# Optimization experiments

Hardware: AMD Instinct MI355X
Metric: run time of the kernel (lower is better)

Reference implementation:

```python
import jax, jax.numpy as jnp
import numpy as np

H = 256  # hidden_size
I = 18   # input_size
B = 1024 # batch
T = 1024 # seq_len


def setup_inputs() -> dict:
    key = jax.random.key(0)
    ks = jax.random.split(key, 8)
    scale = 1.0 / np.sqrt(H)  # matches torch GRUCell uniform init scale roughly
    s = lambda k, shape: jax.random.normal(k, shape, dtype=jnp.float32) * scale
    return {
        "x": jax.random.normal(ks[0], (B, T, I), dtype=jnp.float32),
        # layer 0 GRUCell params (gate order r, z, n as in torch)
        "W_ih0": s(ks[1], (3 * H, I)),
        "W_hh0": s(ks[2], (3 * H, H)),
        "b_ih0": jnp.zeros((3 * H,), dtype=jnp.float32),
        "b_hh0": jnp.zeros((3 * H,), dtype=jnp.float32),
        # layer 1 GRUCell params
        "W_ih1": s(ks[3], (3 * H, H)),
        "W_hh1": s(ks[4], (3 * H, H)),
        "b_ih1": jnp.zeros((3 * H,), dtype=jnp.float32),
        "b_hh1": jnp.zeros((3 * H,), dtype=jnp.float32),
        "fc_w": s(ks[5], (1, H)),
        "fc_b": jnp.zeros((1,), dtype=jnp.float32),
    }


def _gru_cell(x, h, W_ih, W_hh, b_ih, b_hh):
    # torch.nn.GRUCell math, gate order (r, z, n)
    gi = x @ W_ih.T + b_ih  # (B, 3H)
    gh = h @ W_hh.T + b_hh  # (B, 3H)
    ir, iz, inn = jnp.split(gi, 3, axis=-1)
    hr, hz, hn = jnp.split(gh, 3, axis=-1)
    r = jax.nn.sigmoid(ir + hr)
    z = jax.nn.sigmoid(iz + hz)
    n = jnp.tanh(inn + r * hn)
    return (1.0 - z) * n + z * h


def reference(x, W_ih0, W_hh0, b_ih0, b_hh0, W_ih1, W_hh1, b_ih1, b_hh1, fc_w, fc_b):
    batch = x.shape[0]
    hid = W_hh0.shape[1]
    h_init = (jnp.zeros((batch, hid), dtype=x.dtype),
              jnp.zeros((batch, hid), dtype=x.dtype))
    xs = jnp.swapaxes(x, 0, 1)  # (T, B, I) for scan over time

    def step(carry, xt):
        h0, h1 = carry
        h0 = _gru_cell(xt, h0, W_ih0, W_hh0, b_ih0, b_hh0)
        h1 = _gru_cell(h0, h1, W_ih1, W_hh1, b_ih1, b_hh1)
        return (h0, h1), None

    (h0, h1), _ = jax.lax.scan(step, h_init, xs)
    return h1 @ fc_w.T + fc_b  # (B, 1)
```

## Files before the change

kernel.cpp:

```cpp
#include <hip/hip_runtime.h>

#define B_ 1024
#define T_ 1024
#define I_ 18
#define H_ 256
#define NCHUNK 16
#define NSLICE 16

typedef _Float16 f16;
typedef _Float16 f16x8 __attribute__((ext_vector_type(8)));
typedef float f32x4 __attribute__((ext_vector_type(4)));

#define MFMA16(a, b, c) __builtin_amdgcn_mfma_f32_16x16x32_f16((a), (b), (c), 0, 0, 0)
#define SB() __builtin_amdgcn_sched_barrier(0)

#define H_SLOT (NCHUNK * 8 * 4 * 512)
#define NFLAGS (NCHUNK * 4 * 32)

struct TrueT { static constexpr bool value = true; };
struct FalseT { static constexpr bool value = false; };

__device__ __forceinline__ int hoff(int chunk, int kt, int m) {
  return (((chunk * 8) + kt) * 4 + m) * 512;
}

__global__ void init_ws(f16* __restrict__ hb, int* __restrict__ flg) {
  int i = blockIdx.x * blockDim.x + threadIdx.x;
  unsigned* p = (unsigned*)hb;
  for (int k = i; k < 3 * H_SLOT; k += gridDim.x * blockDim.x) p[k] = 0u;
  if (i < NFLAGS + 256 + 1) flg[i] = 0;
}

__device__ __forceinline__ float sigm(float v) {
  return __builtin_amdgcn_rcpf(1.f + __expf(-v));
}
__device__ __forceinline__ float tanh_fast(float v) {
  v = fmaxf(v, -15.f);
  float e = __expf(-2.f * v);
  return (1.f - e) * __builtin_amdgcn_rcpf(1.f + e);
}
__device__ __forceinline__ f16x8 cvt8(const float* q) {
  const f32x4* a = (const f32x4*)q;
  f32x4 u = a[0], v = a[1];
  f16x8 r;
  r[0] = (f16)u[0]; r[1] = (f16)u[1]; r[2] = (f16)u[2]; r[3] = (f16)u[3];
  r[4] = (f16)v[0]; r[5] = (f16)v[1]; r[6] = (f16)v[2]; r[7] = (f16)v[3];
  return r;
}

template <bool FAST>
__device__ __forceinline__ f16x8 ldh(const f16* p) {
  f16x8 r;
  if (FAST)
    asm volatile("global_load_dwordx4 %0, %1, off nt" : "=&v"(r) : "v"(p));
  else
    asm volatile("global_load_dwordx4 %0, %1, off sc0 sc1" : "=&v"(r) : "v"(p));
  return r;
}
template <bool FAST>
__device__ __forceinline__ void sth(f16* p, f16 v) {
  unsigned u = (unsigned)__builtin_bit_cast(unsigned short, v);
  if (FAST)
    asm volatile("global_store_short %0, %1, off" ::"v"(p), "v"(u) : "memory");
  else
    asm volatile("global_store_short %0, %1, off sc0 sc1" ::"v"(p), "v"(u)
                 : "memory");
}
template <bool FAST>
__device__ __forceinline__ void stf(int* p, int v) {
  if (FAST)
    asm volatile("global_store_dword %0, %1, off" ::"v"(p), "v"(v) : "memory");
  else
    asm volatile("global_store_dword %0, %1, off sc0 sc1" ::"v"(p), "v"(v)
                 : "memory");
}
template <bool FAST>
__device__ __forceinline__ int ldf(const int* p) {
  int r;
  if (FAST)
    asm volatile("global_load_dword %0, %1, off nt\n\ts_waitcnt vmcnt(0)"
                 : "=&v"(r) : "v"(p) : "memory");
  else
    asm volatile("global_load_dword %0, %1, off sc0 sc1\n\ts_waitcnt vmcnt(0)"
                 : "=&v"(r) : "v"(p) : "memory");
  return r;
}
__device__ __forceinline__ int ld_sys(const int* p) {
  int r;
  asm volatile("global_load_dword %0, %1, off sc0 sc1\n\ts_waitcnt vmcnt(0)"
               : "=&v"(r) : "v"(p) : "memory");
  return r;
}
__device__ __forceinline__ void st_sys(int* p, int v) { stf<false>(p, v); }
__device__ __forceinline__ f32x4 ldx4(const float* p) {
  f32x4 r;
  asm volatile("global_load_dwordx4 %0, %1, off" : "=&v"(r) : "v"(p));
  return r;
}

__global__ __launch_bounds__(512, 2) void gru_main(
    const float* __restrict__ x, const float* __restrict__ Wih0,
    const float* __restrict__ Whh0, const float* __restrict__ Wih1,
    const float* __restrict__ Whh1, const float* __restrict__ bih0,
    const float* __restrict__ bhh0, const float* __restrict__ bih1,
    const float* __restrict__ bhh1, const float* __restrict__ fcw,
    f16* __restrict__ hb0, f16* __restrict__ hb1, float* __restrict__ part,
    int* __restrict__ flags, int* __restrict__ ids, int* __restrict__ dec) {
  __shared__ f16 whh1_l[24 * 512];

  const int tid = threadIdx.x;
  const int wv = tid >> 6, lane = tid & 63;
  const int w = wv & 3;
  const bool isL0 = wv < 4;
  const int lrow = lane & 15, lgrp = lane >> 4;
  const int chunk = blockIdx.x & 15, slice = blockIdx.x >> 4;
  const int c = slice * 16 + lrow;

  for (int idx = tid; idx < 24 * 64; idx += 512) {
    int f = idx >> 6, l = idx & 63;
    int g = f >> 3, kt = f & 7;
    int n = g * H_ + slice * 16 + (l & 15);
    ((f16x8*)whh1_l)[idx] = cvt8(&Whh1[n * H_ + kt * 32 + (l >> 4) * 8]);
  }

  const int* fpoll = flags + (chunk * 4 + w) * 32 + (lane & 31);
  const int rbase = chunk * 64 + w * 16;
  const int s_kt = slice >> 1;
  const int s_off = 128 * ((slice & 1) * 2 + (lrow >> 3)) + (lrow & 7);

  {
    unsigned xcc;
    asm volatile("s_getreg_b32 %0, hwreg(HW_REG_XCC_ID)" : "=s"(xcc));
    if (tid == 0) st_sys(ids + blockIdx.x, (int)xcc + 1);
    if (blockIdx.x == 0 && wv == 0) {
      int ok, guard = 0;
      for (;;) {
        int v0 = ld_sys(ids + lane * 4 + 0), v1 = ld_sys(ids + lane * 4 + 1);
        int v2 = ld_sys(ids + lane * 4 + 2), v3 = ld_sys(ids + lane * 4 + 3);
        ok = (v0 && v1 && v2 && v3);
        if (__all(ok)) { ok = 1; break; }
        if (++guard > (1 << 16)) { ok = 0; break; }
        __builtin_amdgcn_s_sleep(8);
      }
      int verdict = 1;
      if (ok) {
        int eq = 1;
        if (lane < 16) {
          int r0 = ld_sys(ids + lane);
          for (int s = 1; s < 16; ++s)
            eq &= (ld_sys(ids + s * 16 + lane) == r0);
        }
        verdict = __all(eq) ? 2 : 1;
      }
      if (lane == 0) st_sys(dec, verdict);
    }
  }
  int decision = 1;
  {
    int g = 0;
    for (;;) {
      int d = ld_sys(dec);
      if (d) { decision = d; break; }
      if (++g > (1 << 20)) break;
      __builtin_amdgcn_s_sleep(8);
    }
  }
  __syncthreads();

  if (isL0) {
    f16x8 wfA[27];
#pragma unroll
    for (int g = 0; g < 3; ++g) {
      int n = g * H_ + c;
      f16 v[8];
#pragma unroll
      for (int j = 0; j < 8; ++j) {
        int k = lgrp * 8 + j;
        v[j] = (k < I_) ? (f16)Wih0[n * I_ + k] : (f16)0.f;
      }
      wfA[g] = *(f16x8*)v;
    }
#pragma unroll
    for (int g = 0; g < 3; ++g)
#pragma unroll
      for (int kt = 0; kt < 8; ++kt)
        wfA[3 + g * 8 + kt] =
            cvt8(&Whh0[(g * H_ + c) * H_ + kt * 32 + lgrp * 8]);

    const float bR0 = bih0[c] + bhh0[c], bZ0 = bih0[H_ + c] + bhh0[H_ + c];
    const float bI0 = bih0[2 * H_ + c], bH0 = bhh0[2 * H_ + c];
    float h0r[4] = {0.f, 0.f, 0.f, 0.f};
    int* fpost0 = flags + (chunk * 4 + w) * 32 + slice;
    const float* xrow = x + (size_t)(rbase + lrow) * T_ * I_;
    const int o1 = (lgrp == 0) ? 0 : (lgrp == 1) ? 8 : (lgrp == 2) ? 14 : 0;
    const int o2 = (lgrp == 0) ? 4 : (lgrp == 1) ? 12 : 0;
    int dead = 0;

    auto loop0 = [&](auto FC) {
      constexpr bool F = decltype(FC)::value;
      asm volatile("s_waitcnt vmcnt(0)" ::: "memory");
      SB();
      f32x4 xA1 = ldx4(xrow + o1);
      f32x4 xA2 = ldx4(xrow + o2);
      asm volatile("s_waitcnt vmcnt(0)" ::: "memory");
      SB();
      for (int p = 0; p < T_; ++p) {
        __builtin_amdgcn_s_setprio(1);
        if (p > 0 && !dead) {
          int guard = 0;
          for (;;) {
            int v = ldf<F>(fpoll);
            int tgt = (lane & 16) ? (p - 3) : p;
            if (__all(v >= tgt)) break;
            if (++guard > (1 << 18)) { dead = 1; break; }
          }
        }
        SB();
        f16x8 ah0[8];
        {
          const f16* b0 = hb0 + (size_t)((p - 1) & 3) * H_SLOT +
                          hoff(chunk, 0, w) + lane * 8;
#pragma unroll
          for (int kt = 0; kt < 8; ++kt) ah0[kt] = ldh<F>(b0 + kt * 2048);
        }
        SB();
        f16x8 ax;
        {
          float s0 = (lgrp == 2) ? xA1[2] : xA1[0];
          float s1 = (lgrp == 2) ? xA1[3] : xA1[1];
          ax[0] = (f16)s0;     ax[1] = (f16)s1;
          ax[2] = (f16)xA1[2]; ax[3] = (f16)xA1[3];
          ax[4] = (f16)xA2[0]; ax[5] = (f16)xA2[1];
          ax[6] = (f16)xA2[2]; ax[7] = (f16)xA2[3];
        }
        f32x4 aR = {bR0, bR0, bR0, bR0}, aZ = {bZ0, bZ0, bZ0, bZ0};
        f32x4 aI = {bI0, bI0, bI0, bI0}, aH = {bH0, bH0, bH0, bH0};
        aR = MFMA16(ax, wfA[0], aR);
        aZ = MFMA16(ax, wfA[1], aZ);
        aI = MFMA16(ax, wfA[2], aI);
        SB();
        asm volatile("s_waitcnt vmcnt(4)" ::: "memory");
        SB();
#pragma unroll
        for (int kt = 0; kt < 4; ++kt) {
          aR = MFMA16(ah0[kt], wfA[3 + kt], aR);
          aZ = MFMA16(ah0[kt], wfA[11 + kt], aZ);
          aH = MFMA16(ah0[kt], wfA[19 + kt], aH);
        }
        SB();
        asm volatile("s_waitcnt vmcnt(0)" ::: "memory");
        SB();
#pragma unroll
        for (int kt = 4; kt < 8; ++kt) {
          aR = MFMA16(ah0[kt], wfA[3 + kt], aR);
          aZ = MFMA16(ah0[kt], wfA[11 + kt], aZ);
          aH = MFMA16(ah0[kt], wfA[19 + kt], aH);
        }
        {
          f16* d0 = hb0 + (size_t)(p & 3) * H_SLOT + hoff(chunk, s_kt, w) +
                    s_off;
#pragma unroll
          for (int i = 0; i < 4; ++i) {
            float rr = sigm(aR[i]);
            float zz = sigm(aZ[i]);
            float nn = tanh_fast(aI[i] + rr * aH[i]);
            h0r[i] = (1.f - zz) * nn + zz * h0r[i];
            sth<F>(d0 + (lgrp * 4 + i) * 8, (f16)h0r[i]);
          }
        }
        {
          int tn = (p + 1 < T_) ? p + 1 : T_ - 1;
          const float* px = xrow + (size_t)tn * I_;
          xA1 = ldx4(px + o1);
          xA2 = ldx4(px + o2);
        }
        SB();
        asm volatile("s_waitcnt vmcnt(2)" ::: "memory");
        SB();
        if (lane == 0) stf<F>(fpost0, p + 1);
        __builtin_amdgcn_s_setprio(0);
      }
    };
    if (decision == 2) loop0(TrueT{});
    else loop0(FalseT{});
  } else {
    f16x8 wfB[24];
#pragma unroll
    for (int g = 0; g < 3; ++g)
#pragma unroll
      for (int kt = 0; kt < 8; ++kt)
        wfB[g * 8 + kt] =
            cvt8(&Wih1[(g * H_ + c) * H_ + kt * 32 + lgrp * 8]);

    const float bR1 = bih1[c] + bhh1[c], bZ1 = bih1[H_ + c] + bhh1[H_ + c];
    const float bI1 = bih1[2 * H_ + c], bH1 = bhh1[2 * H_ + c];
    const float fw = fcw[c];
    float h1r[4] = {0.f, 0.f, 0.f, 0.f};
    int* fpost1 = flags + (chunk * 4 + w) * 32 + 16 + slice;
    int dead = 0;

    auto loop1 = [&](auto FC) {
      constexpr bool F = decltype(FC)::value;
      for (int p = 1; p <= T_; ++p) {
        if (!dead) {
          int guard = 0;
          for (;;) {
            int v = ldf<F>(fpoll);
            if (__all((lane & 16) ? (v >= p - 1) : 1)) break;
            if (++guard > (1 << 18)) { dead = 1; break; }
          }
        }
        SB();
        f16x8 ah1[8];
        {
          const f16* b1 = hb1 + (size_t)(p & 1) * H_SLOT +
                          hoff(chunk, 0, w) + lane * 8;
#pragma unroll
          for (int kt = 0; kt < 8; ++kt) ah1[kt] = ldh<F>(b1 + kt * 2048);
        }
        SB();
        if (!dead) {
          int guard = 0;
          for (;;) {
            int v = ldf<F>(fpoll);
            if (__all((lane & 16) ? 1 : (v >= p))) break;
            if (++guard > (1 << 18)) { dead = 1; break; }
          }
        }
        SB();
        f16x8 ah0[8];
        {
          const f16* b0 = hb0 + (size_t)((p - 1) & 3) * H_SLOT +
                          hoff(chunk, 0, w) + lane * 8;
#pragma unroll
          for (int kt = 0; kt < 8; ++kt) ah0[kt] = ldh<F>(b0 + kt * 2048);
        }
        SB();
        f32x4 aR = {bR1, bR1, bR1, bR1}, aZ = {bZ1, bZ1, bZ1, bZ1};
        f32x4 aI = {bI1, bI1, bI1, bI1}, aH = {bH1, bH1, bH1, bH1};
#pragma unroll
        for (int kt = 0; kt < 8; ++kt) {
          f16x8 br = *(const f16x8*)&whh1_l[(0 * 8 + kt) * 512 + lane * 8];
          f16x8 bz = *(const f16x8*)&whh1_l[(1 * 8 + kt) * 512 + lane * 8];
          f16x8 bn = *(const f16x8*)&whh1_l[(2 * 8 + kt) * 512 + lane * 8];
          aR = MFMA16(ah1[kt], br, aR);
          aZ = MFMA16(ah1[kt], bz, aZ);
          aH = MFMA16(ah1[kt], bn, aH);
        }
        SB();
        asm volatile("s_waitcnt vmcnt(0)" ::: "memory");
        SB();
#pragma unroll
        for (int kt = 0; kt < 8; ++kt) {
          aR = MFMA16(ah0[kt], wfB[kt], aR);
          aZ = MFMA16(ah0[kt], wfB[8 + kt], aZ);
          aI = MFMA16(ah0[kt], wfB[16 + kt], aI);
        }
        {
          f16* d1 = hb1 + (size_t)((p - 1) & 1) * H_SLOT +
                    hoff(chunk, s_kt, w) + s_off;
#pragma unroll
          for (int i = 0; i < 4; ++i) {
            float rr = sigm(aR[i]);
            float zz = sigm(aZ[i]);
            float nn = tanh_fast(aI[i] + rr * aH[i]);
            h1r[i] = (1.f - zz) * nn + zz * h1r[i];
            sth<F>(d1 + (lgrp * 4 + i) * 8, (f16)h1r[i]);
          }
        }
        SB();
        asm volatile("s_waitcnt vmcnt(0)" ::: "memory");
        SB();
        if (lane == 0) stf<F>(fpost1, p);
      }
    };
    if (decision == 2) loop1(TrueT{});
    else loop1(FalseT{});

    float tmp[4];
#pragma unroll
    for (int i = 0; i < 4; ++i) {
      float v = h1r[i] * fw;
#pragma unroll
      for (int m = 1; m < 16; m <<= 1) v += __shfl_xor(v, m);
      tmp[i] = v;
    }
    if (lrow == 0) {
#pragma unroll
      for (int i = 0; i < 4; ++i)
        part[(size_t)(rbase + lgrp * 4 + i) * 16 + slice] = tmp[i];
    }
  }
}

__global__ void fc_reduce(const float* __restrict__ part,
                          const float* __restrict__ fcb,
                          float* __restrict__ out) {
  int r = blockIdx.x * blockDim.x + threadIdx.x;
  if (r < B_) {
    float s = fcb[0];
#pragma unroll
    for (int i = 0; i < 16; ++i) s += part[r * 16 + i];
    out[r] = s;
  }
}

extern "C" void kernel_launch(void* const* d_in, const int* in_sizes, int n_in,
                              void* d_out, int out_size, void* d_ws, size_t ws_size,
                              hipStream_t stream) {
  const float* x    = (const float*)d_in[0];
  const float* Wih0 = (const float*)d_in[1];
  const float* Whh0 = (const float*)d_in[2];
  const float* bih0 = (const float*)d_in[3];
  const float* bhh0 = (const float*)d_in[4];
  const float* Wih1 = (const float*)d_in[5];
  const float* Whh1 = (const float*)d_in[6];
  const float* bih1 = (const float*)d_in[7];
  const float* bhh1 = (const float*)d_in[8];
  const float* fcw  = (const float*)d_in[9];
  const float* fcb  = (const float*)d_in[10];

  f16* hb0 = (f16*)d_ws;
  f16* hb1 = hb0 + (size_t)4 * H_SLOT;
  float* part = (float*)(hb1 + (size_t)2 * H_SLOT);
  int* flags = (int*)(part + 1024 * 16);
  int* ids = flags + NFLAGS;
  int* dec = ids + 256;

  init_ws<<<1024, 256, 0, stream>>>(hb0, flags);
  gru_main<<<256, 512, 0, stream>>>(x, Wih0, Whh0, Wih1, Whh1, bih0, bhh0,
                                    bih1, bhh1, fcw, hb0, hb1, part, flags,
                                    ids, dec);
  fc_reduce<<<4, 256, 0, stream>>>(part, fcb, (float*)d_out);
}
```

Baseline: 1.905 ms.

## Split GRU into three pipelined stages with batch-chunked blocks and LDS-resident hidden state

Replaces the layer-0/layer-1 split over 16 batch chunks × 16 hidden slices with 192 blocks in three stages per 16-row batch chunk. Stage 0 runs the layer-0 recurrence, stage 1 the layer-1 input projection, stage 2 the layer-1 recurrence. Each block now owns the full hidden dimension for its batch rows. The recurrent hidden state stays in an LDS ring instead of being exchanged through global memory every step, and the recurrent weights are split between registers and LDS. Stages hand off through global ring buffers with flag-based credit flow control, and the FC head is fused into the last stage. This removes the per-step global h exchange and the separate reduction kernel, but adds inter-stage latency and leaves one block per CU with higher register pressure.

```diff
diff --git a/kernel.cpp b/kernel.cpp
--- a/kernel.cpp
+++ b/kernel.cpp
@@ -1,34 +1,26 @@
 #include <hip/hip_runtime.h>
 
-#define B_ 1024
 #define T_ 1024
 #define I_ 18
-#define H_ 256
-#define NCHUNK 16
-#define NSLICE 16
+#define NCH 64
+#define GUARD (1 << 18)
 
 typedef _Float16 f16;
 typedef _Float16 f16x8 __attribute__((ext_vector_type(8)));
+typedef _Float16 f16x4 __attribute__((ext_vector_type(4)));
 typedef float f32x4 __attribute__((ext_vector_type(4)));
 
 #define MFMA16(a, b, c) __builtin_amdgcn_mfma_f32_16x16x32_f16((a), (b), (c), 0, 0, 0)
 #define SB() __builtin_amdgcn_sched_barrier(0)
 
-#define H_SLOT (NCHUNK * 8 * 4 * 512)
-#define NFLAGS (NCHUNK * 4 * 32)
-
-struct TrueT { static constexpr bool value = true; };
-struct FalseT { static constexpr bool value = false; };
-
-__device__ __forceinline__ int hoff(int chunk, int kt, int m) {
-  return (((chunk * 8) + kt) * 4 + m) * 512;
-}
-
-__global__ void init_ws(f16* __restrict__ hb, int* __restrict__ flg) {
+#define HB0_ELEMS (4 * 64 * 4096)
+#define GB1_ELEMS (4 * 64 * 12288)
+#define NFLAGS (NCH * 32)
+#define LDS_BYTES 114688
+
+__global__ void init_ws(int* __restrict__ flg) {
   int i = blockIdx.x * blockDim.x + threadIdx.x;
-  unsigned* p = (unsigned*)hb;
-  for (int k = i; k < 3 * H_SLOT; k += gridDim.x * blockDim.x) p[k] = 0u;
-  if (i < NFLAGS + 256 + 1) flg[i] = 0;
+  if (i < NFLAGS + 192 + 1) flg[i] = 0;
 }
 
 __device__ __forceinline__ float sigm(float v) {
@@ -51,28 +43,31 @@
 template <bool FAST>
 __device__ __forceinline__ f16x8 ldh(const f16* p) {
   f16x8 r;
-  if (FAST)
-    asm volatile("global_load_dwordx4 %0, %1, off nt" : "=&v"(r) : "v"(p));
-  else
-    asm volatile("global_load_dwordx4 %0, %1, off sc0 sc1" : "=&v"(r) : "v"(p));
+  if (FAST) asm volatile("global_load_dwordx4 %0, %1, off nt" : "=&v"(r) : "v"(p));
+  else asm volatile("global_load_dwordx4 %0, %1, off sc0 sc1" : "=&v"(r) : "v"(p));
   return r;
 }
 template <bool FAST>
-__device__ __forceinline__ void sth(f16* p, f16 v) {
-  unsigned u = (unsigned)__builtin_bit_cast(unsigned short, v);
-  if (FAST)
-    asm volatile("global_store_short %0, %1, off" ::"v"(p), "v"(u) : "memory");
-  else
-    asm volatile("global_store_short %0, %1, off sc0 sc1" ::"v"(p), "v"(u)
-                 : "memory");
+__device__ __forceinline__ f16x4 ldg8(const f16* p) {
+  f16x4 r;
+  if (FAST) asm volatile("global_load_dwordx2 %0, %1, off nt" : "=&v"(r) : "v"(p));
+  else asm volatile("global_load_dwordx2 %0, %1, off sc0 sc1" : "=&v"(r) : "v"(p));
+  return r;
+}
+template <bool FAST>
+__device__ __forceinline__ void stg16(f16* p, f16x8 v) {
+  if (FAST) asm volatile("global_store_dwordx4 %0, %1, off" ::"v"(p), "v"(v) : "memory");
+  else asm volatile("global_store_dwordx4 %0, %1, off sc0 sc1" ::"v"(p), "v"(v) : "memory");
+}
+template <bool FAST>
+__device__ __forceinline__ void stg8(f16* p, f16x4 v) {
+  if (FAST) asm volatile("global_store_dwordx2 %0, %1, off" ::"v"(p), "v"(v) : "memory");
+  else asm volatile("global_store_dwordx2 %0, %1, off sc0 sc1" ::"v"(p), "v"(v) : "memory");
 }
 template <bool FAST>
 __device__ __forceinline__ void stf(int* p, int v) {
-  if (FAST)
-    asm volatile("global_store_dword %0, %1, off" ::"v"(p), "v"(v) : "memory");
-  else
-    asm volatile("global_store_dword %0, %1, off sc0 sc1" ::"v"(p), "v"(v)
-                 : "memory");
+  if (FAST) asm volatile("global_store_dword %0, %1, off" ::"v"(p), "v"(v) : "memory");
+  else asm volatile("global_store_dword %0, %1, off sc0 sc1" ::"v"(p), "v"(v) : "memory");
 }
 template <bool FAST>
 __device__ __forceinline__ int ldf(const int* p) {
@@ -85,6 +80,11 @@
                  : "=&v"(r) : "v"(p) : "memory");
   return r;
 }
+template <bool FAST>
+__device__ __forceinline__ void ldf_nw(const int* p, int* dst) {
+  if (FAST) asm volatile("global_load_dword %0, %1, off nt" : "=&v"(*dst) : "v"(p) : "memory");
+  else asm volatile("global_load_dword %0, %1, off sc0 sc1" : "=&v"(*dst) : "v"(p) : "memory");
+}
 __device__ __forceinline__ int ld_sys(const int* p) {
   int r;
   asm volatile("global_load_dword %0, %1, off sc0 sc1\n\ts_waitcnt vmcnt(0)"
@@ -98,35 +98,44 @@
   return r;
 }
 
-__global__ __launch_bounds__(512, 2) void gru_main(
+__global__ __launch_bounds__(512, 1) void gru_main(
     const float* __restrict__ x, const float* __restrict__ Wih0,
     const float* __restrict__ Whh0, const float* __restrict__ Wih1,
     const float* __restrict__ Whh1, const float* __restrict__ bih0,
     const float* __restrict__ bhh0, const float* __restrict__ bih1,
     const float* __restrict__ bhh1, const float* __restrict__ fcw,
-    f16* __restrict__ hb0, f16* __restrict__ hb1, float* __restrict__ part,
-    int* __restrict__ flags, int* __restrict__ ids, int* __restrict__ dec) {
-  __shared__ f16 whh1_l[24 * 512];
+    const float* __restrict__ fcb, f16* __restrict__ hb0,
+    f16* __restrict__ gb1, int* __restrict__ flags, int* __restrict__ ids,
+    int* __restrict__ dec, float* __restrict__ out) {
+  extern __shared__ f16 lds[];
+  f16* hring = lds + 96 * 512;
 
   const int tid = threadIdx.x;
   const int wv = tid >> 6, lane = tid & 63;
-  const int w = wv & 3;
-  const bool isL0 = wv < 4;
   const int lrow = lane & 15, lgrp = lane >> 4;
-  const int chunk = blockIdx.x & 15, slice = blockIdx.x >> 4;
-  const int c = slice * 16 + lrow;
-
-  for (int idx = tid; idx < 24 * 64; idx += 512) {
-    int f = idx >> 6, l = idx & 63;
-    int g = f >> 3, kt = f & 7;
-    int n = g * H_ + slice * 16 + (l & 15);
-    ((f16x8*)whh1_l)[idx] = cvt8(&Whh1[n * H_ + kt * 32 + (l >> 4) * 8]);
+  const int stage = blockIdx.x >> 6;
+  const int c = blockIdx.x & 63;
+
+  const float* Wm = (stage == 0) ? Whh0 : (stage == 1) ? Wih1 : Whh1;
+
+  for (int idx = tid; idx < 96 * 64; idx += 512) {
+    int f = idx >> 6, lf = idx & 63;
+    int nt = f >> 1, kk = 6 + (f & 1);
+    *(f16x8*)&lds[f * 512 + lf * 8] =
+        cvt8(&Wm[(nt * 16 + (lf & 15)) * 256 + kk * 32 + (lf >> 4) * 8]);
   }
-
-  const int* fpoll = flags + (chunk * 4 + w) * 32 + (lane & 31);
-  const int rbase = chunk * 64 + w * 16;
-  const int s_kt = slice >> 1;
-  const int s_off = 128 * ((slice & 1) * 2 + (lrow >> 3)) + (lrow & 7);
+  for (int idx = tid; idx < 2 * 4096; idx += 512) hring[idx] = (f16)0.f;
+
+  f16x8 wfr[36];
+#pragma unroll
+  for (int g = 0; g < 3; ++g)
+#pragma unroll
+    for (int tt = 0; tt < 2; ++tt) {
+      int row = g * 256 + 32 * wv + 16 * tt + lrow;
+#pragma unroll
+      for (int kt = 0; kt < 6; ++kt)
+        wfr[(g * 2 + tt) * 6 + kt] = cvt8(&Wm[row * 256 + kt * 32 + lgrp * 8]);
+    }
 
   {
     unsigned xcc;
@@ -135,21 +144,18 @@
     if (blockIdx.x == 0 && wv == 0) {
       int ok, guard = 0;
       for (;;) {
-        int v0 = ld_sys(ids + lane * 4 + 0), v1 = ld_sys(ids + lane * 4 + 1);
-        int v2 = ld_sys(ids + lane * 4 + 2), v3 = ld_sys(ids + lane * 4 + 3);
-        ok = (v0 && v1 && v2 && v3);
+        int v0 = ld_sys(ids + lane), v1 = ld_sys(ids + 64 + lane);
+        int v2 = ld_sys(ids + 128 + lane);
+        ok = (v0 && v1 && v2);
         if (__all(ok)) { ok = 1; break; }
         if (++guard > (1 << 16)) { ok = 0; break; }
         __builtin_amdgcn_s_sleep(8);
       }
       int verdict = 1;
       if (ok) {
-        int eq = 1;
-        if (lane < 16) {
-          int r0 = ld_sys(ids + lane);
-          for (int s = 1; s < 16; ++s)
-            eq &= (ld_sys(ids + s * 16 + lane) == r0);
-        }
+        int r0 = ld_sys(ids + lane), r1 = ld_sys(ids + 64 + lane);
+        int r2 = ld_sys(ids + 128 + lane);
+        int eq = (r1 == r0) && (r2 == r0);
         verdict = __all(eq) ? 2 : 1;
       }
       if (lane == 0) st_sys(dec, verdict);
@@ -167,62 +173,46 @@
   }
   __syncthreads();
 
-  if (isL0) {
-    f16x8 wfA[27];
-#pragma unroll
-    for (int g = 0; g < 3; ++g) {
-      int n = g * H_ + c;
-      f16 v[8];
-#pragma unroll
-      for (int j = 0; j < 8; ++j) {
-        int k = lgrp * 8 + j;
-        v[j] = (k < I_) ? (f16)Wih0[n * I_ + k] : (f16)0.f;
+  int dead = 0;
+
+  if (stage == 0) {
+    f16x8 wx[6];
+#pragma unroll
+    for (int g = 0; g < 3; ++g)
+#pragma unroll
+      for (int tt = 0; tt < 2; ++tt) {
+        int row = g * 256 + 32 * wv + 16 * tt + lrow;
+        f16 v[8];
+#pragma unroll
+        for (int j = 0; j < 8; ++j) {
+          int k = lgrp * 8 + j;
+          v[j] = (k < I_) ? (f16)Wih0[row * I_ + k] : (f16)0.f;
+        }
+        wx[g * 2 + tt] = *(f16x8*)v;
       }
-      wfA[g] = *(f16x8*)v;
-    }
-#pragma unroll
-    for (int g = 0; g < 3; ++g)
-#pragma unroll
-      for (int kt = 0; kt < 8; ++kt)
-        wfA[3 + g * 8 + kt] =
-            cvt8(&Whh0[(g * H_ + c) * H_ + kt * 32 + lgrp * 8]);
-
-    const float bR0 = bih0[c] + bhh0[c], bZ0 = bih0[H_ + c] + bhh0[H_ + c];
-    const float bI0 = bih0[2 * H_ + c], bH0 = bhh0[2 * H_ + c];
-    float h0r[4] = {0.f, 0.f, 0.f, 0.f};
-    int* fpost0 = flags + (chunk * 4 + w) * 32 + slice;
-    const float* xrow = x + (size_t)(rbase + lrow) * T_ * I_;
+    float bR[2], bZ[2], bI[2], bH[2];
+#pragma unroll
+    for (int tt = 0; tt < 2; ++tt) {
+      int col = 32 * wv + 16 * tt + lrow;
+      bR[tt] = bih0[col] + bhh0[col];
+      bZ[tt] = bih0[256 + col] + bhh0[256 + col];
+      bI[tt] = bih0[512 + col];
+      bH[tt] = bhh0[512 + col];
+    }
+    float h0r[2][4] = {{0.f, 0.f, 0.f, 0.f}, {0.f, 0.f, 0.f, 0.f}};
+    const float* xrow = x + (size_t)(c * 16 + lrow) * T_ * I_;
     const int o1 = (lgrp == 0) ? 0 : (lgrp == 1) ? 8 : (lgrp == 2) ? 14 : 0;
     const int o2 = (lgrp == 0) ? 4 : (lgrp == 1) ? 12 : 0;
-    int dead = 0;
+    int* fpost = flags + c * 32 + 0 * 8 + wv;
+    const int* fcred = flags + c * 32 + 2 * 8 + (lane & 7);
+    int cval = 0;
 
     auto loop0 = [&](auto FC) {
       constexpr bool F = decltype(FC)::value;
-      asm volatile("s_waitcnt vmcnt(0)" ::: "memory");
-      SB();
       f32x4 xA1 = ldx4(xrow + o1);
       f32x4 xA2 = ldx4(xrow + o2);
-      asm volatile("s_waitcnt vmcnt(0)" ::: "memory");
-      SB();
-      for (int p = 0; p < T_; ++p) {
-        __builtin_amdgcn_s_setprio(1);
-        if (p > 0 && !dead) {
-          int guard = 0;
-          for (;;) {
-            int v = ldf<F>(fpoll);
-            int tgt = (lane & 16) ? (p - 3) : p;
-            if (__all(v >= tgt)) break;
-            if (++guard > (1 << 18)) { dead = 1; break; }
-          }
-        }
-        SB();
-        f16x8 ah0[8];
-        {
-          const f16* b0 = hb0 + (size_t)((p - 1) & 3) * H_SLOT +
-                          hoff(chunk, 0, w) + lane * 8;
-#pragma unroll
-          for (int kt = 0; kt < 8; ++kt) ah0[kt] = ldh<F>(b0 + kt * 2048);
-        }
+      for (int t = 0; t < T_; ++t) {
+        asm volatile("s_waitcnt vmcnt(2)" ::: "memory");
         SB();
         f16x8 ax;
         {
@@ -233,175 +223,260 @@
           ax[4] = (f16)xA2[0]; ax[5] = (f16)xA2[1];
           ax[6] = (f16)xA2[2]; ax[7] = (f16)xA2[3];
         }
-        f32x4 aR = {bR0, bR0, bR0, bR0}, aZ = {bZ0, bZ0, bZ0, bZ0};
-        f32x4 aI = {bI0, bI0, bI0, bI0}, aH = {bH0, bH0, bH0, bH0};
-        aR = MFMA16(ax, wfA[0], aR);
-        aZ = MFMA16(ax, wfA[1], aZ);
-        aI = MFMA16(ax, wfA[2], aI);
-        SB();
-        asm volatile("s_waitcnt vmcnt(4)" ::: "memory");
-        SB();
-#pragma unroll
-        for (int kt = 0; kt < 4; ++kt) {
-          aR = MFMA16(ah0[kt], wfA[3 + kt], aR);
-          aZ = MFMA16(ah0[kt], wfA[11 + kt], aZ);
-          aH = MFMA16(ah0[kt], wfA[19 + kt], aH);
-        }
-        SB();
+        f32x4 aR[2], aZ[2], aI[2], aH[2];
+#pragma unroll
+        for (int tt = 0; tt < 2; ++tt) {
+          aR[tt] = (f32x4){bR[tt], bR[tt], bR[tt], bR[tt]};
+          aZ[tt] = (f32x4){bZ[tt], bZ[tt], bZ[tt], bZ[tt]};
+          aI[tt] = (f32x4){bI[tt], bI[tt], bI[tt], bI[tt]};
+          aH[tt] = (f32x4){bH[tt], bH[tt], bH[tt], bH[tt]};
+          aR[tt] = MFMA16(ax, wx[0 * 2 + tt], aR[tt]);
+          aZ[tt] = MFMA16(ax, wx[1 * 2 + tt], aZ[tt]);
+          aI[tt] = MFMA16(ax, wx[2 * 2 + tt], aI[tt]);
+        }
+        const f16* ha = &hring[((t + 1) & 1) * 4096 + lane * 8];
+#pragma unroll
+        for (int kt = 0; kt < 8; ++kt) {
+          f16x8 a = *(const f16x8*)(ha + kt * 512);
+#pragma unroll
+          for (int tt = 0; tt < 2; ++tt) {
+            f16x8 br = (kt < 6) ? wfr[(0 * 2 + tt) * 6 + kt]
+                : *(const f16x8*)&lds[(((0 * 16 + wv * 2 + tt) * 2) + (kt - 6)) * 512 + lane * 8];
+            f16x8 bz = (kt < 6) ? wfr[(1 * 2 + tt) * 6 + kt]
+                : *(const f16x8*)&lds[(((1 * 16 + wv * 2 + tt) * 2) + (kt - 6)) * 512 + lane * 8];
+            f16x8 bn = (kt < 6) ? wfr[(2 * 2 + tt) * 6 + kt]
+                : *(const f16x8*)&lds[(((2 * 16 + wv * 2 + tt) * 2) + (kt - 6)) * 512 + lane * 8];
+            aR[tt] = MFMA16(a, br, aR[tt]);
+            aZ[tt] = MFMA16(a, bz, aZ[tt]);
+            aH[tt] = MFMA16(a, bn, aH[tt]);
+          }
+        }
+#pragma unroll
+        for (int tt = 0; tt < 2; ++tt)
+#pragma unroll
+          for (int i = 0; i < 4; ++i) {
+            float rr = sigm(aR[tt][i]);
+            float zz = sigm(aZ[tt][i]);
+            float nn = tanh_fast(aI[tt][i] + rr * aH[tt][i]);
+            h0r[tt][i] = (1.f - zz) * nn + zz * h0r[tt][i];
+            int off = wv * 512 + ((lgrp * 4 + i) + 16 * (2 * tt + (lrow >> 3))) * 8 + (lrow & 7);
+            hring[(t & 1) * 4096 + off] = (f16)h0r[tt][i];
+          }
+        f16x8 own = *(const f16x8*)&hring[(t & 1) * 4096 + wv * 512 + lane * 8];
         asm volatile("s_waitcnt vmcnt(0)" ::: "memory");
         SB();
-#pragma unroll
-        for (int kt = 4; kt < 8; ++kt) {
-          aR = MFMA16(ah0[kt], wfA[3 + kt], aR);
-          aZ = MFMA16(ah0[kt], wfA[11 + kt], aZ);
-          aH = MFMA16(ah0[kt], wfA[19 + kt], aH);
-        }
+        if (t >= 4 && !dead) {
+          if (!__all(cval >= t - 3)) {
+            int guard = 0;
+            for (;;) {
+              int v = ldf<F>(fcred);
+              if (__all(v >= t - 3)) break;
+              if (++guard > GUARD) { dead = 1; break; }
+            }
+          }
+        }
+        stg16<F>(hb0 + (size_t)(((t & 3) * 64 + c) * 8 + wv) * 512 + lane * 8, own);
         {
-          f16* d0 = hb0 + (size_t)(p & 3) * H_SLOT + hoff(chunk, s_kt, w) +
-                    s_off;
-#pragma unroll
-          for (int i = 0; i < 4; ++i) {
-            float rr = sigm(aR[i]);
-            float zz = sigm(aZ[i]);
-            float nn = tanh_fast(aI[i] + rr * aH[i]);
-            h0r[i] = (1.f - zz) * nn + zz * h0r[i];
-            sth<F>(d0 + (lgrp * 4 + i) * 8, (f16)h0r[i]);
-          }
-        }
-        {
-          int tn = (p + 1 < T_) ? p + 1 : T_ - 1;
-          const float* px = xrow + (size_t)tn * I_;
-          xA1 = ldx4(px + o1);
-          xA2 = ldx4(px + o2);
-        }
-        SB();
+          int tn = (t + 1 < T_) ? t + 1 : T_ - 1;
+          xA1 = ldx4(xrow + (size_t)tn * I_ + o1);
+          xA2 = ldx4(xrow + (size_t)tn * I_ + o2);
+        }
+        __syncthreads();
         asm volatile("s_waitcnt vmcnt(2)" ::: "memory");
         SB();
-        if (lane == 0) stf<F>(fpost0, p + 1);
-        __builtin_amdgcn_s_setprio(0);
+        if (lane == 0) stf<F>(fpost, t + 1);
+        ldf_nw<F>(fcred, &cval);
       }
     };
-    if (decision == 2) loop0(TrueT{});
-    else loop0(FalseT{});
-  } else {
-    f16x8 wfB[24];
-#pragma unroll
-    for (int g = 0; g < 3; ++g)
-#pragma unroll
-      for (int kt = 0; kt < 8; ++kt)
-        wfB[g * 8 + kt] =
-            cvt8(&Wih1[(g * H_ + c) * H_ + kt * 32 + lgrp * 8]);
-
-    const float bR1 = bih1[c] + bhh1[c], bZ1 = bih1[H_ + c] + bhh1[H_ + c];
-    const float bI1 = bih1[2 * H_ + c], bH1 = bhh1[2 * H_ + c];
-    const float fw = fcw[c];
-    float h1r[4] = {0.f, 0.f, 0.f, 0.f};
-    int* fpost1 = flags + (chunk * 4 + w) * 32 + 16 + slice;
-    int dead = 0;
+    if (decision == 2) loop0(std::integral_constant<bool, true>{});
+    else loop0(std::integral_constant<bool, false>{});
+  } else if (stage == 1) {
+    float bR[2], bZ[2], bI[2];
+#pragma unroll
+    for (int tt = 0; tt < 2; ++tt) {
+      int col = 32 * wv + 16 * tt + lrow;
+      bR[tt] = bih1[col];
+      bZ[tt] = bih1[256 + col];
+      bI[tt] = bih1[512 + col];
+    }
+    const int* fh0p = flags + c * 32 + 0 * 8 + (lane & 7);
+    const int* fcred = flags + c * 32 + 3 * 8 + (lane & 7);
+    int* fpost_p = flags + c * 32 + 2 * 8 + wv;
+    int* fpost_d = flags + c * 32 + 1 * 8 + wv;
 
     auto loop1 = [&](auto FC) {
       constexpr bool F = decltype(FC)::value;
-      for (int p = 1; p <= T_; ++p) {
+      for (int t = 0; t < T_; ++t) {
+        if (t >= 4 && !dead) {
+          int guard = 0;
+          for (;;) {
+            int v = ldf<F>(fcred);
+            if (__all(v >= t - 3)) break;
+            if (++guard > GUARD) { dead = 1; break; }
+          }
+        }
         if (!dead) {
           int guard = 0;
           for (;;) {
-            int v = ldf<F>(fpoll);
-            if (__all((lane & 16) ? (v >= p - 1) : 1)) break;
-            if (++guard > (1 << 18)) { dead = 1; break; }
-          }
-        }
-        SB();
-        f16x8 ah1[8];
-        {
-          const f16* b1 = hb1 + (size_t)(p & 1) * H_SLOT +
-                          hoff(chunk, 0, w) + lane * 8;
-#pragma unroll
-          for (int kt = 0; kt < 8; ++kt) ah1[kt] = ldh<F>(b1 + kt * 2048);
-        }
-        SB();
+            int v = ldf<F>(fh0p);
+            if (__all(v >= t + 1)) break;
+            if (++guard > GUARD) { dead = 1; break; }
+          }
+        }
+        SB();
+        const f16* hb = hb0 + (size_t)((t & 3) * 64 + c) * 4096 + lane * 8;
+        f16x8 ah[8];
+#pragma unroll
+        for (int kt = 0; kt < 8; ++kt) ah[kt] = ldh<F>(hb + kt * 512);
+        SB();
+        f32x4 aR[2], aZ[2], aI[2];
+#pragma unroll
+        for (int tt = 0; tt < 2; ++tt) {
+          aR[tt] = (f32x4){bR[tt], bR[tt], bR[tt], bR[tt]};
+          aZ[tt] = (f32x4){bZ[tt], bZ[tt], bZ[tt], bZ[tt]};
+          aI[tt] = (f32x4){bI[tt], bI[tt], bI[tt], bI[tt]};
+        }
+        asm volatile("s_waitcnt vmcnt(4)" ::: "memory");
+        SB();
+#pragma unroll
+        for (int kt = 0; kt < 4; ++kt)
+#pragma unroll
+          for (int tt = 0; tt < 2; ++tt) {
+            f16x8 br = (kt < 6) ? wfr[(0 * 2 + tt) * 6 + kt] : ah[0];
+            aR[tt] = MFMA16(ah[kt], wfr[(0 * 2 + tt) * 6 + kt], aR[tt]);
+            aZ[tt] = MFMA16(ah[kt], wfr[(1 * 2 + tt) * 6 + kt], aZ[tt]);
+            aI[tt] = MFMA16(ah[kt], wfr[(2 * 2 + tt) * 6 + kt], aI[tt]);
+            (void)br;
+          }
+        asm volatile("s_waitcnt vmcnt(0)" ::: "memory");
+        SB();
+        if (lane == 0) stf<F>(fpost_p, t + 1);
+#pragma unroll
+        for (int kt = 4; kt < 8; ++kt)
+#pragma unroll
+          for (int tt = 0; tt < 2; ++tt) {
+            f16x8 br = (kt < 6) ? wfr[(0 * 2 + tt) * 6 + kt]
+                : *(const f16x8*)&lds[(((0 * 16 + wv * 2 + tt) * 2) + (kt - 6)) * 512 + lane * 8];
+            f16x8 bz = (kt < 6) ? wfr[(1 * 2 + tt) * 6 + kt]
+                : *(const f16x8*)&lds[(((1 * 16 + wv * 2 + tt) * 2) + (kt - 6)) * 512 + lane * 8];
+            f16x8 bn = (kt < 6) ? wfr[(2 * 2 + tt) * 6 + kt]
+                : *(const f16x8*)&lds[(((2 * 16 + wv * 2 + tt) * 2) + (kt - 6)) * 512 + lane * 8];
+            aR[tt] = MFMA16(ah[kt], br, aR[tt]);
+            aZ[tt] = MFMA16(ah[kt], bz, aZ[tt]);
+            aI[tt] = MFMA16(ah[kt], bn, aI[tt]);
+          }
+        f16* gbase = gb1 + (size_t)((t & 3) * 64 + c) * 12288 + lane * 4;
+#pragma unroll
+        for (int g = 0; g < 3; ++g)
+#pragma unroll
+          for (int tt = 0; tt < 2; ++tt) {
+            int nt = g * 16 + wv * 2 + tt;
+            f32x4 a = (g == 0) ? aR[tt] : (g == 1) ? aZ[tt] : aI[tt];
+            f16x4 v;
+            v[0] = (f16)a[0]; v[1] = (f16)a[1]; v[2] = (f16)a[2]; v[3] = (f16)a[3];
+            stg8<F>(gbase + nt * 256, v);
+          }
+        asm volatile("s_waitcnt vmcnt(0)" ::: "memory");
+        SB();
+        if (lane == 0) stf<F>(fpost_d, t + 1);
+      }
+    };
+    if (decision == 2) loop1(std::integral_constant<bool, true>{});
+    else loop1(std::integral_constant<bool, false>{});
+  } else {
+    float bR[2], bZ[2], bH[2];
+#pragma unroll
+    for (int tt = 0; tt < 2; ++tt) {
+      int col = 32 * wv + 16 * tt + lrow;
+      bR[tt] = bhh1[col];
+      bZ[tt] = bhh1[256 + col];
+      bH[tt] = bhh1[512 + col];
+    }
+    float h1r[2][4] = {{0.f, 0.f, 0.f, 0.f}, {0.f, 0.f, 0.f, 0.f}};
+    const int* fgip = flags + c * 32 + 1 * 8 + (lane & 7);
+    int* fpost = flags + c * 32 + 3 * 8 + wv;
+
+    auto loop2 = [&](auto FC) {
+      constexpr bool F = decltype(FC)::value;
+      for (int t = 0; t < T_; ++t) {
         if (!dead) {
           int guard = 0;
           for (;;) {
-            int v = ldf<F>(fpoll);
-            if (__all((lane & 16) ? 1 : (v >= p))) break;
-            if (++guard > (1 << 18)) { dead = 1; break; }
-          }
-        }
-        SB();
-        f16x8 ah0[8];
-        {
-          const f16* b0 = hb0 + (size_t)((p - 1) & 3) * H_SLOT +
-                          hoff(chunk, 0, w) + lane * 8;
-#pragma unroll
-          for (int kt = 0; kt < 8; ++kt) ah0[kt] = ldh<F>(b0 + kt * 2048);
-        }
-        SB();
-        f32x4 aR = {bR1, bR1, bR1, bR1}, aZ = {bZ1, bZ1, bZ1, bZ1};
-        f32x4 aI = {bI1, bI1, bI1, bI1}, aH = {bH1, bH1, bH1, bH1};
+            int v = ldf<F>(fgip);
+            if (__all(v >= t + 1)) break;
+            if (++guard > GUARD) { dead = 1; break; }
+          }
+        }
+        SB();
+        const f16* gbase = gb1 + (size_t)((t & 3) * 64 + c) * 12288 + lane * 4;
+        f16x4 gi[6];
+#pragma unroll
+        for (int g = 0; g < 3; ++g)
+#pragma unroll
+          for (int tt = 0; tt < 2; ++tt)
+            gi[g * 2 + tt] = ldg8<F>(gbase + (g * 16 + wv * 2 + tt) * 256);
+        SB();
+        f32x4 aR[2], aZ[2], aH[2];
+#pragma unroll
+        for (int tt = 0; tt < 2; ++tt) {
+          aR[tt] = (f32x4){bR[tt], bR[tt], bR[tt], bR[tt]};
+          aZ[tt] = (f32x4){bZ[tt], bZ[tt], bZ[tt], bZ[tt]};
+          aH[tt] = (f32x4){bH[tt], bH[tt], bH[tt], bH[tt]};
+        }
+        const f16* ha = &hring[((t + 1) & 1) * 4096 + lane * 8];
 #pragma unroll
         for (int kt = 0; kt < 8; ++kt) {
-          f16x8 br = *(const f16x8*)&whh1_l[(0 * 8 + kt) * 512 + lane * 8];
-          f16x8 bz = *(const f16x8*)&whh1_l[(1 * 8 + kt) * 512 + lane * 8];
-          f16x8 bn = *(const f16x8*)&whh1_l[(2 * 8 + kt) * 512 + lane * 8];
-          aR = MFMA16(ah1[kt], br, aR);
-          aZ = MFMA16(ah1[kt], bz, aZ);
-          aH = MFMA16(ah1[kt], bn, aH);
-        }
-        SB();
+          f16x8 a = *(const f16x8*)(ha + kt * 512);
+#pragma unroll
+          for (int tt = 0; tt < 2; ++tt) {
+            f16x8 br = (kt < 6) ? wfr[(0 * 2 + tt) * 6 + kt]
+                : *(const f16x8*)&lds[(((0 * 16 + wv * 2 + tt) * 2) + (kt - 6)) * 512 + lane * 8];
+            f16x8 bz = (kt < 6) ? wfr[(1 * 2 + tt) * 6 + kt]
+                : *(const f16x8*)&lds[(((1 * 16 + wv * 2 + tt) * 2) + (kt - 6)) * 512 + lane * 8];
+            f16x8 bn = (kt < 6) ? wfr[(2 * 2 + tt) * 6 + kt]
+                : *(const f16x8*)&lds[(((2 * 16 + wv * 2 + tt) * 2) + (kt - 6)) * 512 + lane * 8];
+            aR[tt] = MFMA16(a, br, aR[tt]);
+            aZ[tt] = MFMA16(a, bz, aZ[tt]);
+            aH[tt] = MFMA16(a, bn, aH[tt]);
+          }
+        }
         asm volatile("s_waitcnt vmcnt(0)" ::: "memory");
         SB();
-#pragma unroll
-        for (int kt = 0; kt < 8; ++kt) {
-          aR = MFMA16(ah0[kt], wfB[kt], aR);
-          aZ = MFMA16(ah0[kt], wfB[8 + kt], aZ);
-          aI = MFMA16(ah0[kt], wfB[16 + kt], aI);
-        }
-        {
-          f16* d1 = hb1 + (size_t)((p - 1) & 1) * H_SLOT +
-                    hoff(chunk, s_kt, w) + s_off;
+        if (lane == 0) stf<F>(fpost, t + 1);
+#pragma unroll
+        for (int tt = 0; tt < 2; ++tt)
 #pragma unroll
           for (int i = 0; i < 4; ++i) {
-            float rr = sigm(aR[i]);
-            float zz = sigm(aZ[i]);
-            float nn = tanh_fast(aI[i] + rr * aH[i]);
-            h1r[i] = (1.f - zz) * nn + zz * h1r[i];
-            sth<F>(d1 + (lgrp * 4 + i) * 8, (f16)h1r[i]);
-          }
-        }
-        SB();
-        asm volatile("s_waitcnt vmcnt(0)" ::: "memory");
-        SB();
-        if (lane == 0) stf<F>(fpost1, p);
+            float rr = sigm((float)gi[0 * 2 + tt][i] + aR[tt][i]);
+            float zz = sigm((float)gi[1 * 2 + tt][i] + aZ[tt][i]);
+            float nn = tanh_fast((float)gi[2 * 2 + tt][i] + rr * aH[tt][i]);
+            h1r[tt][i] = (1.f - zz) * nn + zz * h1r[tt][i];
+            int off = wv * 512 + ((lgrp * 4 + i) + 16 * (2 * tt + (lrow >> 3))) * 8 + (lrow & 7);
+            hring[(t & 1) * 4096 + off] = (f16)h1r[tt][i];
+          }
+        __syncthreads();
       }
     };
-    if (decision == 2) loop1(TrueT{});
-    else loop1(FalseT{});
-
-    float tmp[4];
+    if (decision == 2) loop2(std::integral_constant<bool, true>{});
+    else loop2(std::integral_constant<bool, false>{});
+
+    float fw0 = fcw[32 * wv + lrow], fw1 = fcw[32 * wv + 16 + lrow];
+    float* red = (float*)lds;
+    __syncthreads();
 #pragma unroll
     for (int i = 0; i < 4; ++i) {
-      float v = h1r[i] * fw;
+      float v = h1r[0][i] * fw0 + h1r[1][i] * fw1;
 #pragma unroll
       for (int m = 1; m < 16; m <<= 1) v += __shfl_xor(v, m);
-      tmp[i] = v;
-    }
-    if (lrow == 0) {
-#pragma unroll
-      for (int i = 0; i < 4; ++i)
-        part[(size_t)(rbase + lgrp * 4 + i) * 16 + slice] = tmp[i];
-    }
-  }
-}
-
-__global__ void fc_reduce(const float* __restrict__ part,
-                          const float* __restrict__ fcb,
-                          float* __restrict__ out) {
-  int r = blockIdx.x * blockDim.x + threadIdx.x;
-  if (r < B_) {
-    float s = fcb[0];
-#pragma unroll
-    for (int i = 0; i < 16; ++i) s += part[r * 16 + i];
-    out[r] = s;
+      if (lrow == 0) red[wv * 16 + lgrp * 4 + i] = v;
+    }
+    __syncthreads();
+    if (tid < 16) {
+      float s = fcb[0];
+#pragma unroll
+      for (int w2 = 0; w2 < 8; ++w2) s += red[w2 * 16 + tid];
+      out[c * 16 + tid] = s;
+    }
   }
 }
 
@@ -421,15 +496,16 @@
   const float* fcb  = (const float*)d_in[10];
 
   f16* hb0 = (f16*)d_ws;
-  f16* hb1 = hb0 + (size_t)4 * H_SLOT;
-  float* part = (float*)(hb1 + (size_t)2 * H_SLOT);
-  int* flags = (int*)(part + 1024 * 16);
+  f16* gb1 = hb0 + (size_t)HB0_ELEMS;
+  int* flags = (int*)(gb1 + (size_t)GB1_ELEMS);
   int* ids = flags + NFLAGS;
-  int* dec = ids + 256;
-
-  init_ws<<<1024, 256, 0, stream>>>(hb0, flags);
-  gru_main<<<256, 512, 0, stream>>>(x, Wih0, Whh0, Wih1, Whh1, bih0, bhh0,
-                                    bih1, bhh1, fcw, hb0, hb1, part, flags,
-                                    ids, dec);
-  fc_reduce<<<4, 256, 0, stream>>>(part, fcb, (float*)d_out);
-}
+  int* dec = ids + 192;
+
+  hipFuncSetAttribute((const void*)gru_main,
+                      hipFuncAttributeMaxDynamicSharedMemorySize, LDS_BYTES);
+
+  init_ws<<<16, 256, 0, stream>>>(flags);
+  gru_main<<<192, 512, LDS_BYTES, stream>>>(
+      x, Wih0, Whh0, Wih1, Whh1, bih0, bhh0, bih1, bhh1, fcw, fcb, hb0, gb1,
+      flags, ids, dec, (float*)d_out);
+}
```

Result: slower. 2.953 ms (+55.0%).
